# Kernel optimization log

Measured on AMD Instinct MI355X. Metric: run time of the kernel, lower is better.

Reference implementation:

```python
import jax, jax.numpy as jnp
import numpy as np

SEQ = 4096
EMB = 1024
OUT = 1024


def setup_inputs() -> dict:
    key = jax.random.key(0)
    k_x, k_q, k_k, k_v = jax.random.split(key, 4)
    scale = 1.0 / np.sqrt(EMB)
    inputs = jax.random.normal(k_x, (SEQ, EMB), dtype=jnp.float32)
    # torch Linear weight is (out_features, in_features); y = x @ W.T
    W_Q = jax.random.normal(k_q, (OUT, EMB), dtype=jnp.float32) * scale
    W_K = jax.random.normal(k_k, (OUT, EMB), dtype=jnp.float32) * scale
    W_V = jax.random.normal(k_v, (OUT, EMB), dtype=jnp.float32) * scale
    return {"inputs": inputs, "W_Q": W_Q, "W_K": W_K, "W_V": W_V}


def reference(inputs, W_Q, W_K, W_V):
    # projections: (S, E) @ (E, D) -> (S, D)
    q = inputs @ W_Q.T
    k = inputs @ W_K.T
    v = inputs @ W_V.T
    d_k = k.shape[-1]
    scores = (q @ k.T) / jnp.sqrt(jnp.asarray(d_k, dtype=q.dtype))  # (S, S)
    weights = jax.nn.softmax(scores, axis=-1)
    return weights @ v  # (S, D)
```

## Files before the change

kernel.cpp:

```cpp
#include <hip/hip_runtime.h>

typedef __bf16 bf16;
typedef __bf16 bf16x4 __attribute__((ext_vector_type(4)));
typedef __bf16 bf16x8 __attribute__((ext_vector_type(8)));
typedef float f32x4 __attribute__((ext_vector_type(4)));

#define SEQ 4096
#define EMB 1024

__device__ __forceinline__ void async_copy16(void* lds, const void* g) {
    __builtin_amdgcn_global_load_lds(
        (const __attribute__((address_space(1))) unsigned int*)g,
        (__attribute__((address_space(3))) unsigned int*)lds,
        16, 0, 0);
}

__global__ __launch_bounds__(256) void prep_all(const float* __restrict__ x,
                                                const float* __restrict__ wq,
                                                const float* __restrict__ wk,
                                                const float* __restrict__ wv,
                                                bf16* __restrict__ xb,
                                                bf16* __restrict__ wqk,
                                                bf16* __restrict__ wvb,
                                                float* __restrict__ rowsum)
{
    const int u = blockIdx.x * 256 + threadIdx.x;
    const float* src;
    bf16* dst;
    int off;
    if (u < 1048576)      { src = x;  dst = xb;               off = u; }
    else if (u < 1310720) { src = wq; dst = wqk;              off = u - 1048576; }
    else if (u < 1572864) { src = wk; dst = wqk + EMB * EMB;  off = u - 1310720; }
    else if (u < 1835008) { src = wv; dst = wvb;              off = u - 1572864; }
    else {
        *(float4*)(rowsum + (size_t)(u - 1835008) * 4) = float4{0.f, 0.f, 0.f, 0.f};
        return;
    }
    float4 f = *(const float4*)(src + (size_t)off * 4);
    bf16x4 v = { (bf16)f.x, (bf16)f.y, (bf16)f.z, (bf16)f.w };
    *(bf16x4*)(dst + (size_t)off * 4) = v;
}

template<bool RSUM>
__device__ __forceinline__ void tile_compute(const bf16* __restrict__ As,
                                             const bf16* __restrict__ Bs,
                                             int wr, int wc, int fr, int q,
                                             f32x4 (&acc)[8][4], float (&rsum)[8],
                                             bool rs_active)
{
    const int pc0 = ((q + fr) & 7) * 8;
    const int pc1 = pc0 ^ 32;

    bf16x8 bg[4][2];
#pragma unroll
    for (int nf = 0; nf < 4; nf++) {
        const bf16* bp = Bs + (wc * 64 + nf * 16 + fr) * 64;
        bg[nf][0] = *(const bf16x8*)(bp + pc0);
        bg[nf][1] = *(const bf16x8*)(bp + pc1);
    }
#pragma unroll
    for (int mg = 0; mg < 2; mg++) {
        bf16x8 af[4][2];
#pragma unroll
        for (int mf = 0; mf < 4; mf++) {
            const bf16* ap = As + (wr * 128 + mg * 64 + mf * 16 + fr) * 64;
            af[mf][0] = *(const bf16x8*)(ap + pc0);
            af[mf][1] = *(const bf16x8*)(ap + pc1);
        }
        if (RSUM && rs_active) {
#pragma unroll
            for (int mf = 0; mf < 4; mf++)
#pragma unroll
                for (int kh = 0; kh < 2; kh++)
#pragma unroll
                    for (int e = 0; e < 8; e++)
                        rsum[mg * 4 + mf] += (float)af[mf][kh][e];
        }
        __builtin_amdgcn_s_setprio(1);
#pragma unroll
        for (int nf = 0; nf < 4; nf++)
#pragma unroll
            for (int mf = 0; mf < 4; mf++) {
                f32x4 c = acc[mg * 4 + mf][nf];
                c = __builtin_amdgcn_mfma_f32_16x16x32_bf16(af[mf][0], bg[nf][0], c, 0, 0, 0);
                c = __builtin_amdgcn_mfma_f32_16x16x32_bf16(af[mf][1], bg[nf][1], c, 0, 0, 0);
                acc[mg * 4 + mf][nf] = c;
            }
        __builtin_amdgcn_s_setprio(0);
    }
}

template<bool RSUM>
__device__ __forceinline__ void gemm_core256(const bf16* __restrict__ A,
                                             const bf16* __restrict__ B,
                                             int lda, int ldb, long koff,
                                             int m0, int n0,
                                             bf16* __restrict__ As,
                                             bf16* __restrict__ Bs,
                                             f32x4 (&acc)[8][4], float (&rsum)[8],
                                             bool rs_active)
{
    const int tid  = threadIdx.x;
    const int lane = tid & 63;
    const int wave = tid >> 6;
    const int wr = wave >> 2;
    const int wc = wave & 3;
    const int srow = tid >> 3;
    const int spc  = tid & 7;
    const int sl   = (spc - (srow & 7)) & 7;
    const int fr = lane & 15;
    const int q  = lane >> 4;

#pragma unroll
    for (int i = 0; i < 8; i++)
#pragma unroll
        for (int j = 0; j < 4; j++) acc[i][j] = {0.f, 0.f, 0.f, 0.f};
    if (RSUM)
#pragma unroll
        for (int i = 0; i < 8; i++) rsum[i] = 0.f;

    const bf16* Ab = A + (size_t)(m0 + srow) * lda + koff + sl * 8;
    const bf16* Bb = B + (size_t)(n0 + srow) * ldb + koff + sl * 8;
    bf16* AsD = As + srow * 64 + spc * 8;
    bf16* BsD = Bs + srow * 64 + spc * 8;

#pragma unroll
    for (int u = 0; u < 4; u++) {
        async_copy16(AsD + u * 4096, Ab + (size_t)(64 * u) * lda);
        async_copy16(BsD + u * 4096, Bb + (size_t)(64 * u) * ldb);
    }

    for (int t = 0; t < 15; t++) {
        const int p = t & 1;
        const long kk = (long)(t + 1) * 64;
#pragma unroll
        for (int u = 0; u < 4; u++) {
            async_copy16(AsD + (1 - p) * 16384 + u * 4096, Ab + kk + (size_t)(64 * u) * lda);
            async_copy16(BsD + (1 - p) * 16384 + u * 4096, Bb + kk + (size_t)(64 * u) * ldb);
        }
        asm volatile("s_waitcnt vmcnt(8)" ::: "memory");
        __builtin_amdgcn_s_barrier();
        tile_compute<RSUM>(As + p * 16384, Bs + p * 16384, wr, wc, fr, q, acc, rsum, rs_active);
        asm volatile("" ::: "memory");
        __builtin_amdgcn_s_barrier();
    }
    asm volatile("s_waitcnt vmcnt(0)" ::: "memory");
    __builtin_amdgcn_s_barrier();
    tile_compute<RSUM>(As + 16384, Bs + 16384, wr, wc, fr, q, acc, rsum, rs_active);
}

__global__ __launch_bounds__(512, 2) void gemm_proj(const bf16* __restrict__ xb,
                                                    const bf16* __restrict__ wqk,
                                                    const bf16* __restrict__ wvb,
                                                    bf16* __restrict__ QK,
                                                    bf16* __restrict__ VT)
{
    __shared__ __align__(16) bf16 As[2][16384];
    __shared__ __align__(16) bf16 Bs[2][16384];

    const bf16 *A, *B;
    bf16* C;
    int ldc, m0, n0;
    if (blockIdx.y < 8) {
        A = xb; B = wqk; C = QK; ldc = 2048;
        m0 = blockIdx.x * 256; n0 = blockIdx.y * 256;
    } else {
        const int id = blockIdx.x + (blockIdx.y - 8) * 16;
        A = wvb; B = xb; C = VT; ldc = 4096;
        m0 = (id & 3) * 256; n0 = (id >> 2) * 256;
    }

    f32x4 acc[8][4];
    float rs[8];
    gemm_core256<false>(A, B, 1024, 1024, 0, m0, n0, &As[0][0], &Bs[0][0], acc, rs, false);

    const int lane = threadIdx.x & 63;
    const int wave = threadIdx.x >> 6;
    const int cm = m0 + (wave >> 2) * 128 + ((lane >> 4) << 2);
    const int cn = n0 + (wave & 3) * 64 + (lane & 15);
#pragma unroll
    for (int i = 0; i < 8; i++)
#pragma unroll
        for (int j = 0; j < 4; j++)
#pragma unroll
            for (int r = 0; r < 4; r++)
                C[(size_t)(cm + i * 16 + r) * ldc + (cn + j * 16)] = (bf16)acc[i][j][r];
}

__global__ __launch_bounds__(512, 2) void gemm_exp(const bf16* __restrict__ QK,
                                                   bf16* __restrict__ E)
{
    __shared__ __align__(16) bf16 As[2][16384];
    __shared__ __align__(16) bf16 Bs[2][16384];

    const int m0 = blockIdx.x * 256;
    const int n0 = blockIdx.y * 256;
    f32x4 acc[8][4];
    float rs[8];
    gemm_core256<false>(QK, QK + 1024, 2048, 2048, 0, m0, n0, &As[0][0], &Bs[0][0], acc, rs, false);

    const int lane = threadIdx.x & 63;
    const int wave = threadIdx.x >> 6;
    const int cm = m0 + (wave >> 2) * 128 + ((lane >> 4) << 2);
    const int cn = n0 + (wave & 3) * 64 + (lane & 15);
#pragma unroll
    for (int i = 0; i < 8; i++)
#pragma unroll
        for (int j = 0; j < 4; j++)
#pragma unroll
            for (int r = 0; r < 4; r++)
                E[(size_t)(cm + i * 16 + r) * 4096 + (cn + j * 16)] =
                    (bf16)__expf(acc[i][j][r] * 0.03125f);
}

__global__ __launch_bounds__(512, 2) void gemm_pv(const bf16* __restrict__ E,
                                                  const bf16* __restrict__ VT,
                                                  float* __restrict__ out,
                                                  float* __restrict__ p1,
                                                  float* __restrict__ rowsum)
{
    __shared__ __align__(16) bf16 As[2][16384];
    __shared__ __align__(16) bf16 Bs[2][16384];

    const int m0 = blockIdx.x * 256;
    const int n0 = blockIdx.y * 256;
    const long koff = (long)blockIdx.z * 1024;
    const bool rs_active = (blockIdx.y == 0) && (((threadIdx.x >> 6) & 3) == 0);

    f32x4 acc[8][4];
    float rs[8];
    gemm_core256<true>(E, VT, 4096, 4096, koff, m0, n0, &As[0][0], &Bs[0][0], acc, rs, rs_active);

    const int lane = threadIdx.x & 63;
    const int wave = threadIdx.x >> 6;
    if (rs_active) {
#pragma unroll
        for (int i = 0; i < 8; i++) {
            rs[i] += __shfl_xor(rs[i], 16);
            rs[i] += __shfl_xor(rs[i], 32);
        }
        if (lane < 16) {
            const int rbase = m0 + (wave >> 2) * 128;
#pragma unroll
            for (int i = 0; i < 8; i++)
                unsafeAtomicAdd(&rowsum[rbase + i * 16 + lane], rs[i]);
        }
    }

    float* C = (blockIdx.z == 0) ? out : p1 + (size_t)(blockIdx.z - 1) * SEQ * 1024;
    const int cm = m0 + (wave >> 2) * 128 + ((lane >> 4) << 2);
    const int cn = n0 + (wave & 3) * 64 + (lane & 15);
#pragma unroll
    for (int i = 0; i < 8; i++)
#pragma unroll
        for (int j = 0; j < 4; j++)
#pragma unroll
            for (int r = 0; r < 4; r++)
                C[(size_t)(cm + i * 16 + r) * 1024 + (cn + j * 16)] = acc[i][j][r];
}

__global__ __launch_bounds__(256) void reduce_norm(float* __restrict__ out,
                                                   const float* __restrict__ p1,
                                                   const float* __restrict__ p2,
                                                   const float* __restrict__ p3,
                                                   const float* __restrict__ rowsum)
{
    const int m = blockIdx.x;
    const float inv = 1.f / rowsum[m];
    const size_t off = (size_t)m * 1024 + threadIdx.x * 4;
    float4 a = *(const float4*)(out + off);
    float4 b = *(const float4*)(p1 + off);
    float4 c = *(const float4*)(p2 + off);
    float4 d = *(const float4*)(p3 + off);
    float4 o;
    o.x = (a.x + b.x + c.x + d.x) * inv;
    o.y = (a.y + b.y + c.y + d.y) * inv;
    o.z = (a.z + b.z + c.z + d.z) * inv;
    o.w = (a.w + b.w + c.w + d.w) * inv;
    *(float4*)(out + off) = o;
}

extern "C" void kernel_launch(void* const* d_in, const int* in_sizes, int n_in,
                              void* d_out, int out_size, void* d_ws, size_t ws_size,
                              hipStream_t stream)
{
    const float* x  = (const float*)d_in[0];
    const float* wq = (const float*)d_in[1];
    const float* wk = (const float*)d_in[2];
    const float* wv = (const float*)d_in[3];
    float* out = (float*)d_out;

    char* ws = (char*)d_ws;
    const size_t MB = 1024 * 1024;
    bf16*  E   = (bf16*)(ws);
    float* p1  = (float*)(ws + 32 * MB);
    float* p2  = (float*)(ws + 48 * MB);
    float* p3  = (float*)(ws + 64 * MB);
    bf16*  xb  = (bf16*)(ws + 32 * MB);
    bf16*  wqk = (bf16*)(ws + 40 * MB);
    bf16*  wvb = (bf16*)(ws + 44 * MB);
    bf16*  QK  = (bf16*)(ws + 64 * MB);
    bf16*  VT  = (bf16*)(ws + 80 * MB);
    float* rsm = (float*)(ws + 88 * MB);

    prep_all<<<dim3(7172), dim3(256), 0, stream>>>(x, wq, wk, wv, xb, wqk, wvb, rsm);
    gemm_proj<<<dim3(16, 12), dim3(512), 0, stream>>>(xb, wqk, wvb, QK, VT);
    gemm_exp<<<dim3(16, 16), dim3(512), 0, stream>>>(QK, E);
    gemm_pv<<<dim3(16, 4, 4), dim3(512), 0, stream>>>(E, VT, out, p1, rsm);
    reduce_norm<<<dim3(4096), dim3(256), 0, stream>>>(out, p1, p2, p3, rsm);
}
```

Measured before the change: 211.4 us.

## Split tile compute into barrier-synchronized quadrant phases with ping-pong scheduling

Restructures the per-k-tile compute into four phases that each load one A or B fragment group from LDS, then run MFMAs on one quadrant of the accumulator tile, with barriers and lgkmcnt waits between phases. The intent is to interleave LDS reads with MFMA work across the two wave groups and lower register pressure by holding only half the A and B fragments at a time. Launch bounds are relaxed from 2 to 1 blocks per CU, which allows more registers per thread but may reduce occupancy. The extra barriers per tile add synchronization overhead.

```diff
diff --git a/kernel.cpp b/kernel.cpp
--- a/kernel.cpp
+++ b/kernel.cpp
@@ -42,52 +42,125 @@
 }
 
 template<bool RSUM>
-__device__ __forceinline__ void tile_compute(const bf16* __restrict__ As,
-                                             const bf16* __restrict__ Bs,
-                                             int wr, int wc, int fr, int q,
-                                             f32x4 (&acc)[8][4], float (&rsum)[8],
-                                             bool rs_active)
+__device__ __forceinline__ void tile_phases(const bf16* __restrict__ Asp,
+                                            const bf16* __restrict__ Bsp,
+                                            int wr, int wc, int fr, int q,
+                                            f32x4 (&acc)[8][4], float (&rsum)[8],
+                                            bool rs_active)
 {
     const int pc0 = ((q + fr) & 7) * 8;
     const int pc1 = pc0 ^ 32;
-
-    bf16x8 bg[4][2];
-#pragma unroll
-    for (int nf = 0; nf < 4; nf++) {
-        const bf16* bp = Bs + (wc * 64 + nf * 16 + fr) * 64;
-        bg[nf][0] = *(const bf16x8*)(bp + pc0);
-        bg[nf][1] = *(const bf16x8*)(bp + pc1);
-    }
-#pragma unroll
-    for (int mg = 0; mg < 2; mg++) {
-        bf16x8 af[4][2];
+    const bf16* aBase = Asp + (wr * 128 + fr) * 64;
+    const bf16* bBase = Bsp + (wc * 64 + fr) * 64;
+
+    bf16x8 af[4][2];
+    bf16x8 bg[2][2][2];
+
+#pragma unroll
+    for (int mf = 0; mf < 4; mf++) {
+        af[mf][0] = *(const bf16x8*)(aBase + (mf * 16) * 64 + pc0);
+        af[mf][1] = *(const bf16x8*)(aBase + (mf * 16) * 64 + pc1);
+    }
+#pragma unroll
+    for (int nj = 0; nj < 2; nj++) {
+        bg[0][nj][0] = *(const bf16x8*)(bBase + (nj * 16) * 64 + pc0);
+        bg[0][nj][1] = *(const bf16x8*)(bBase + (nj * 16) * 64 + pc1);
+    }
+    asm volatile("" ::: "memory");
+    __builtin_amdgcn_s_barrier();
+    asm volatile("s_waitcnt lgkmcnt(0)" ::: "memory");
+    __builtin_amdgcn_sched_barrier(0);
+    __builtin_amdgcn_s_setprio(1);
+#pragma unroll
+    for (int nj = 0; nj < 2; nj++)
 #pragma unroll
         for (int mf = 0; mf < 4; mf++) {
-            const bf16* ap = As + (wr * 128 + mg * 64 + mf * 16 + fr) * 64;
-            af[mf][0] = *(const bf16x8*)(ap + pc0);
-            af[mf][1] = *(const bf16x8*)(ap + pc1);
-        }
-        if (RSUM && rs_active) {
-#pragma unroll
-            for (int mf = 0; mf < 4; mf++)
-#pragma unroll
-                for (int kh = 0; kh < 2; kh++)
-#pragma unroll
-                    for (int e = 0; e < 8; e++)
-                        rsum[mg * 4 + mf] += (float)af[mf][kh][e];
-        }
-        __builtin_amdgcn_s_setprio(1);
-#pragma unroll
-        for (int nf = 0; nf < 4; nf++)
-#pragma unroll
-            for (int mf = 0; mf < 4; mf++) {
-                f32x4 c = acc[mg * 4 + mf][nf];
-                c = __builtin_amdgcn_mfma_f32_16x16x32_bf16(af[mf][0], bg[nf][0], c, 0, 0, 0);
-                c = __builtin_amdgcn_mfma_f32_16x16x32_bf16(af[mf][1], bg[nf][1], c, 0, 0, 0);
-                acc[mg * 4 + mf][nf] = c;
-            }
-        __builtin_amdgcn_s_setprio(0);
-    }
+            f32x4 c = acc[mf][nj];
+            c = __builtin_amdgcn_mfma_f32_16x16x32_bf16(af[mf][0], bg[0][nj][0], c, 0, 0, 0);
+            c = __builtin_amdgcn_mfma_f32_16x16x32_bf16(af[mf][1], bg[0][nj][1], c, 0, 0, 0);
+            acc[mf][nj] = c;
+        }
+    __builtin_amdgcn_s_setprio(0);
+    if (RSUM && rs_active) {
+#pragma unroll
+        for (int mf = 0; mf < 4; mf++)
+#pragma unroll
+            for (int kh = 0; kh < 2; kh++)
+#pragma unroll
+                for (int e = 0; e < 8; e++)
+                    rsum[mf] += (float)af[mf][kh][e];
+    }
+    asm volatile("" ::: "memory");
+    __builtin_amdgcn_s_barrier();
+
+#pragma unroll
+    for (int nj = 0; nj < 2; nj++) {
+        bg[1][nj][0] = *(const bf16x8*)(bBase + ((2 + nj) * 16) * 64 + pc0);
+        bg[1][nj][1] = *(const bf16x8*)(bBase + ((2 + nj) * 16) * 64 + pc1);
+    }
+    asm volatile("" ::: "memory");
+    __builtin_amdgcn_s_barrier();
+    asm volatile("s_waitcnt lgkmcnt(0)" ::: "memory");
+    __builtin_amdgcn_sched_barrier(0);
+    __builtin_amdgcn_s_setprio(1);
+#pragma unroll
+    for (int nj = 0; nj < 2; nj++)
+#pragma unroll
+        for (int mf = 0; mf < 4; mf++) {
+            f32x4 c = acc[mf][2 + nj];
+            c = __builtin_amdgcn_mfma_f32_16x16x32_bf16(af[mf][0], bg[1][nj][0], c, 0, 0, 0);
+            c = __builtin_amdgcn_mfma_f32_16x16x32_bf16(af[mf][1], bg[1][nj][1], c, 0, 0, 0);
+            acc[mf][2 + nj] = c;
+        }
+    __builtin_amdgcn_s_setprio(0);
+    asm volatile("" ::: "memory");
+    __builtin_amdgcn_s_barrier();
+
+#pragma unroll
+    for (int mf = 0; mf < 4; mf++) {
+        af[mf][0] = *(const bf16x8*)(aBase + (64 + mf * 16) * 64 + pc0);
+        af[mf][1] = *(const bf16x8*)(aBase + (64 + mf * 16) * 64 + pc1);
+    }
+    asm volatile("" ::: "memory");
+    __builtin_amdgcn_s_barrier();
+    asm volatile("s_waitcnt lgkmcnt(0)" ::: "memory");
+    __builtin_amdgcn_sched_barrier(0);
+    __builtin_amdgcn_s_setprio(1);
+#pragma unroll
+    for (int nj = 0; nj < 2; nj++)
+#pragma unroll
+        for (int mf = 0; mf < 4; mf++) {
+            f32x4 c = acc[4 + mf][2 + nj];
+            c = __builtin_amdgcn_mfma_f32_16x16x32_bf16(af[mf][0], bg[1][nj][0], c, 0, 0, 0);
+            c = __builtin_amdgcn_mfma_f32_16x16x32_bf16(af[mf][1], bg[1][nj][1], c, 0, 0, 0);
+            acc[4 + mf][2 + nj] = c;
+        }
+    __builtin_amdgcn_s_setprio(0);
+    if (RSUM && rs_active) {
+#pragma unroll
+        for (int mf = 0; mf < 4; mf++)
+#pragma unroll
+            for (int kh = 0; kh < 2; kh++)
+#pragma unroll
+                for (int e = 0; e < 8; e++)
+                    rsum[4 + mf] += (float)af[mf][kh][e];
+    }
+    asm volatile("" ::: "memory");
+    __builtin_amdgcn_s_barrier();
+
+    __builtin_amdgcn_s_setprio(1);
+#pragma unroll
+    for (int nj = 0; nj < 2; nj++)
+#pragma unroll
+        for (int mf = 0; mf < 4; mf++) {
+            f32x4 c = acc[4 + mf][nj];
+            c = __builtin_amdgcn_mfma_f32_16x16x32_bf16(af[mf][0], bg[0][nj][0], c, 0, 0, 0);
+            c = __builtin_amdgcn_mfma_f32_16x16x32_bf16(af[mf][1], bg[0][nj][1], c, 0, 0, 0);
+            acc[4 + mf][nj] = c;
+        }
+    __builtin_amdgcn_s_setprio(0);
+    asm volatile("" ::: "memory");
+    __builtin_amdgcn_s_barrier();
 }
 
 template<bool RSUM>
@@ -140,16 +213,14 @@
         }
         asm volatile("s_waitcnt vmcnt(8)" ::: "memory");
         __builtin_amdgcn_s_barrier();
-        tile_compute<RSUM>(As + p * 16384, Bs + p * 16384, wr, wc, fr, q, acc, rsum, rs_active);
-        asm volatile("" ::: "memory");
-        __builtin_amdgcn_s_barrier();
+        tile_phases<RSUM>(As + p * 16384, Bs + p * 16384, wr, wc, fr, q, acc, rsum, rs_active);
     }
     asm volatile("s_waitcnt vmcnt(0)" ::: "memory");
     __builtin_amdgcn_s_barrier();
-    tile_compute<RSUM>(As + 16384, Bs + 16384, wr, wc, fr, q, acc, rsum, rs_active);
-}
-
-__global__ __launch_bounds__(512, 2) void gemm_proj(const bf16* __restrict__ xb,
+    tile_phases<RSUM>(As + 16384, Bs + 16384, wr, wc, fr, q, acc, rsum, rs_active);
+}
+
+__global__ __launch_bounds__(512, 1) void gemm_proj(const bf16* __restrict__ xb,
                                                     const bf16* __restrict__ wqk,
                                                     const bf16* __restrict__ wvb,
                                                     bf16* __restrict__ QK,
@@ -187,7 +258,7 @@
                 C[(size_t)(cm + i * 16 + r) * ldc + (cn + j * 16)] = (bf16)acc[i][j][r];
 }
 
-__global__ __launch_bounds__(512, 2) void gemm_exp(const bf16* __restrict__ QK,
+__global__ __launch_bounds__(512, 1) void gemm_exp(const bf16* __restrict__ QK,
                                                    bf16* __restrict__ E)
 {
     __shared__ __align__(16) bf16 As[2][16384];
@@ -213,7 +284,7 @@
                     (bf16)__expf(acc[i][j][r] * 0.03125f);
 }
 
-__global__ __launch_bounds__(512, 2) void gemm_pv(const bf16* __restrict__ E,
+__global__ __launch_bounds__(512, 1) void gemm_pv(const bf16* __restrict__ E,
                                                   const bf16* __restrict__ VT,
                                                   float* __restrict__ out,
                                                   float* __restrict__ p1,
```

New measurement: 226.9 us. 1.07x slower.

## Restructure GEMM mainloop into 4-stage K=32 pipeline with register ping-pong

Applied to the files above, without the earlier changes.

Replaces the double-buffered K=64 GEMM loop with a four-buffer K=32 pipeline. It prefetches two tiles ahead, splits the A and B async copies around the barrier, and double-buffers the B fragments in registers so LDS reads overlap the MFMA work. Launch bounds drop from 2 to 1 blocks per CU because shared memory use doubles. The aim is to hide global and LDS latency behind the matrix math, at the cost of occupancy and finer-grained waitcnt tuning that could stall if the counts are wrong.

```diff
diff --git a/kernel.cpp b/kernel.cpp
--- a/kernel.cpp
+++ b/kernel.cpp
@@ -42,51 +42,88 @@
 }
 
 template<bool RSUM>
-__device__ __forceinline__ void tile_compute(const bf16* __restrict__ As,
-                                             const bf16* __restrict__ Bs,
-                                             int wr, int wc, int fr, int q,
-                                             f32x4 (&acc)[8][4], float (&rsum)[8],
-                                             bool rs_active)
-{
-    const int pc0 = ((q + fr) & 7) * 8;
-    const int pc1 = pc0 ^ 32;
-
-    bf16x8 bg[4][2];
-#pragma unroll
-    for (int nf = 0; nf < 4; nf++) {
-        const bf16* bp = Bs + (wc * 64 + nf * 16 + fr) * 64;
-        bg[nf][0] = *(const bf16x8*)(bp + pc0);
-        bg[nf][1] = *(const bf16x8*)(bp + pc1);
-    }
-#pragma unroll
-    for (int mg = 0; mg < 2; mg++) {
-        bf16x8 af[4][2];
-#pragma unroll
-        for (int mf = 0; mf < 4; mf++) {
-            const bf16* ap = As + (wr * 128 + mg * 64 + mf * 16 + fr) * 64;
-            af[mf][0] = *(const bf16x8*)(ap + pc0);
-            af[mf][1] = *(const bf16x8*)(ap + pc1);
-        }
-        if (RSUM && rs_active) {
+__device__ __forceinline__ void tile_step(int t, int NT,
+                                          const bf16* __restrict__ Ab,
+                                          const bf16* __restrict__ Bb,
+                                          int lda, int ldb,
+                                          bf16* __restrict__ As,
+                                          bf16* __restrict__ Bs,
+                                          bf16* __restrict__ AsD,
+                                          bf16* __restrict__ BsD,
+                                          int wr, int wc, int fr, int pc,
+                                          bf16x8 (&afA)[4], bf16x8 (&afB)[4],
+                                          bf16x8 (&bgC)[4], bf16x8 (&bgN)[4],
+                                          f32x4 (&acc)[8][4], float (&rsum)[8],
+                                          bool rs_active)
+{
+    if (t + 2 < NT) {
+        const int b2 = ((t + 2) & 3) * 8192;
+        async_copy16(AsD + b2,        Ab + (t + 2) * 32);
+        async_copy16(AsD + b2 + 4096, Ab + (t + 2) * 32 + (size_t)128 * lda);
+    }
+    {
+        const bf16* At = As + (t & 3) * 8192 + (wr * 128 + 64 + fr) * 32 + pc;
+#pragma unroll
+        for (int mf = 0; mf < 4; mf++)
+            afB[mf] = *(const bf16x8*)(At + (mf * 16) * 32);
+    }
+    asm volatile("s_waitcnt lgkmcnt(4)" ::: "memory");
+    __builtin_amdgcn_sched_barrier(0);
+    __builtin_amdgcn_s_setprio(1);
+#pragma unroll
+    for (int nj = 0; nj < 4; nj++)
+#pragma unroll
+        for (int mf = 0; mf < 4; mf++)
+            acc[mf][nj] = __builtin_amdgcn_mfma_f32_16x16x32_bf16(afA[mf], bgC[nj], acc[mf][nj], 0, 0, 0);
+    __builtin_amdgcn_s_setprio(0);
+    if (RSUM && rs_active) {
+#pragma unroll
+        for (int mf = 0; mf < 4; mf++)
+#pragma unroll
+            for (int e = 0; e < 8; e++) rsum[mf] += (float)afA[mf][e];
+    }
+
+    if (t < NT - 1) {
+        if (t + 2 < NT) {
+            asm volatile("s_waitcnt vmcnt(2)" ::: "memory");
+        } else {
+            asm volatile("s_waitcnt vmcnt(0)" ::: "memory");
+        }
+        __builtin_amdgcn_s_barrier();
+        if (t + 2 < NT) {
+            const int b2 = ((t + 2) & 3) * 8192;
+            async_copy16(BsD + b2,        Bb + (t + 2) * 32);
+            async_copy16(BsD + b2 + 4096, Bb + (t + 2) * 32 + (size_t)128 * ldb);
+        }
+        {
+            const int b1 = ((t + 1) & 3) * 8192;
+            const bf16* At = As + b1 + (wr * 128 + fr) * 32 + pc;
+            const bf16* Bt = Bs + b1 + (wc * 64 + fr) * 32 + pc;
 #pragma unroll
             for (int mf = 0; mf < 4; mf++)
-#pragma unroll
-                for (int kh = 0; kh < 2; kh++)
-#pragma unroll
-                    for (int e = 0; e < 8; e++)
-                        rsum[mg * 4 + mf] += (float)af[mf][kh][e];
-        }
-        __builtin_amdgcn_s_setprio(1);
-#pragma unroll
-        for (int nf = 0; nf < 4; nf++)
-#pragma unroll
-            for (int mf = 0; mf < 4; mf++) {
-                f32x4 c = acc[mg * 4 + mf][nf];
-                c = __builtin_amdgcn_mfma_f32_16x16x32_bf16(af[mf][0], bg[nf][0], c, 0, 0, 0);
-                c = __builtin_amdgcn_mfma_f32_16x16x32_bf16(af[mf][1], bg[nf][1], c, 0, 0, 0);
-                acc[mg * 4 + mf][nf] = c;
-            }
-        __builtin_amdgcn_s_setprio(0);
+                afA[mf] = *(const bf16x8*)(At + (mf * 16) * 32);
+#pragma unroll
+            for (int nj = 0; nj < 4; nj++)
+                bgN[nj] = *(const bf16x8*)(Bt + (nj * 16) * 32);
+        }
+        asm volatile("s_waitcnt lgkmcnt(8)" ::: "memory");
+        __builtin_amdgcn_sched_barrier(0);
+    } else {
+        asm volatile("s_waitcnt lgkmcnt(0)" ::: "memory");
+        __builtin_amdgcn_sched_barrier(0);
+    }
+    __builtin_amdgcn_s_setprio(1);
+#pragma unroll
+    for (int nj = 0; nj < 4; nj++)
+#pragma unroll
+        for (int mf = 0; mf < 4; mf++)
+            acc[4 + mf][nj] = __builtin_amdgcn_mfma_f32_16x16x32_bf16(afB[mf], bgC[nj], acc[4 + mf][nj], 0, 0, 0);
+    __builtin_amdgcn_s_setprio(0);
+    if (RSUM && rs_active) {
+#pragma unroll
+        for (int mf = 0; mf < 4; mf++)
+#pragma unroll
+            for (int e = 0; e < 8; e++) rsum[4 + mf] += (float)afB[mf][e];
     }
 }
 
@@ -105,11 +142,13 @@
     const int wave = tid >> 6;
     const int wr = wave >> 2;
     const int wc = wave & 3;
-    const int srow = tid >> 3;
-    const int spc  = tid & 7;
-    const int sl   = (spc - (srow & 7)) & 7;
+    const int srow = tid >> 2;
+    const int spc  = tid & 3;
+    const int sl   = (spc - (srow & 3)) & 3;
     const int fr = lane & 15;
     const int q  = lane >> 4;
+    const int pc = ((q + fr) & 3) * 8;
+    const int NT = 32;
 
 #pragma unroll
     for (int i = 0; i < 8; i++)
@@ -121,42 +160,47 @@
 
     const bf16* Ab = A + (size_t)(m0 + srow) * lda + koff + sl * 8;
     const bf16* Bb = B + (size_t)(n0 + srow) * ldb + koff + sl * 8;
-    bf16* AsD = As + srow * 64 + spc * 8;
-    bf16* BsD = Bs + srow * 64 + spc * 8;
-
-#pragma unroll
-    for (int u = 0; u < 4; u++) {
-        async_copy16(AsD + u * 4096, Ab + (size_t)(64 * u) * lda);
-        async_copy16(BsD + u * 4096, Bb + (size_t)(64 * u) * ldb);
-    }
-
-    for (int t = 0; t < 15; t++) {
-        const int p = t & 1;
-        const long kk = (long)(t + 1) * 64;
-#pragma unroll
-        for (int u = 0; u < 4; u++) {
-            async_copy16(AsD + (1 - p) * 16384 + u * 4096, Ab + kk + (size_t)(64 * u) * lda);
-            async_copy16(BsD + (1 - p) * 16384 + u * 4096, Bb + kk + (size_t)(64 * u) * ldb);
-        }
-        asm volatile("s_waitcnt vmcnt(8)" ::: "memory");
-        __builtin_amdgcn_s_barrier();
-        tile_compute<RSUM>(As + p * 16384, Bs + p * 16384, wr, wc, fr, q, acc, rsum, rs_active);
-        asm volatile("" ::: "memory");
-        __builtin_amdgcn_s_barrier();
-    }
-    asm volatile("s_waitcnt vmcnt(0)" ::: "memory");
+    bf16* AsD = As + srow * 32 + spc * 8;
+    bf16* BsD = Bs + srow * 32 + spc * 8;
+
+#pragma unroll
+    for (int tt = 0; tt < 2; tt++) {
+        async_copy16(AsD + tt * 8192,        Ab + tt * 32);
+        async_copy16(AsD + tt * 8192 + 4096, Ab + tt * 32 + (size_t)128 * lda);
+        async_copy16(BsD + tt * 8192,        Bb + tt * 32);
+        async_copy16(BsD + tt * 8192 + 4096, Bb + tt * 32 + (size_t)128 * ldb);
+    }
+    asm volatile("s_waitcnt vmcnt(4)" ::: "memory");
     __builtin_amdgcn_s_barrier();
-    tile_compute<RSUM>(As + 16384, Bs + 16384, wr, wc, fr, q, acc, rsum, rs_active);
-}
-
-__global__ __launch_bounds__(512, 2) void gemm_proj(const bf16* __restrict__ xb,
+
+    bf16x8 afA[4], afB[4], bg0[4], bg1[4];
+    {
+        const bf16* At = As + (wr * 128 + fr) * 32 + pc;
+        const bf16* Bt = Bs + (wc * 64 + fr) * 32 + pc;
+#pragma unroll
+        for (int mf = 0; mf < 4; mf++)
+            afA[mf] = *(const bf16x8*)(At + (mf * 16) * 32);
+#pragma unroll
+        for (int nj = 0; nj < 4; nj++)
+            bg0[nj] = *(const bf16x8*)(Bt + (nj * 16) * 32);
+    }
+
+    for (int t = 0; t < NT; t += 2) {
+        tile_step<RSUM>(t,     NT, Ab, Bb, lda, ldb, As, Bs, AsD, BsD,
+                        wr, wc, fr, pc, afA, afB, bg0, bg1, acc, rsum, rs_active);
+        tile_step<RSUM>(t + 1, NT, Ab, Bb, lda, ldb, As, Bs, AsD, BsD,
+                        wr, wc, fr, pc, afA, afB, bg1, bg0, acc, rsum, rs_active);
+    }
+}
+
+__global__ __launch_bounds__(512, 1) void gemm_proj(const bf16* __restrict__ xb,
                                                     const bf16* __restrict__ wqk,
                                                     const bf16* __restrict__ wvb,
                                                     bf16* __restrict__ QK,
                                                     bf16* __restrict__ VT)
 {
-    __shared__ __align__(16) bf16 As[2][16384];
-    __shared__ __align__(16) bf16 Bs[2][16384];
+    __shared__ __align__(16) bf16 As[4][8192];
+    __shared__ __align__(16) bf16 Bs[4][8192];
 
     const bf16 *A, *B;
     bf16* C;
@@ -187,11 +231,11 @@
                 C[(size_t)(cm + i * 16 + r) * ldc + (cn + j * 16)] = (bf16)acc[i][j][r];
 }
 
-__global__ __launch_bounds__(512, 2) void gemm_exp(const bf16* __restrict__ QK,
+__global__ __launch_bounds__(512, 1) void gemm_exp(const bf16* __restrict__ QK,
                                                    bf16* __restrict__ E)
 {
-    __shared__ __align__(16) bf16 As[2][16384];
-    __shared__ __align__(16) bf16 Bs[2][16384];
+    __shared__ __align__(16) bf16 As[4][8192];
+    __shared__ __align__(16) bf16 Bs[4][8192];
 
     const int m0 = blockIdx.x * 256;
     const int n0 = blockIdx.y * 256;
@@ -213,14 +257,14 @@
                     (bf16)__expf(acc[i][j][r] * 0.03125f);
 }
 
-__global__ __launch_bounds__(512, 2) void gemm_pv(const bf16* __restrict__ E,
+__global__ __launch_bounds__(512, 1) void gemm_pv(const bf16* __restrict__ E,
                                                   const bf16* __restrict__ VT,
                                                   float* __restrict__ out,
                                                   float* __restrict__ p1,
                                                   float* __restrict__ rowsum)
 {
-    __shared__ __align__(16) bf16 As[2][16384];
-    __shared__ __align__(16) bf16 Bs[2][16384];
+    __shared__ __align__(16) bf16 As[4][8192];
+    __shared__ __align__(16) bf16 Bs[4][8192];
 
     const int m0 = blockIdx.x * 256;
     const int n0 = blockIdx.y * 256;
```

After: 207.9 us. Within noise of the previous version (-1.7%).

## Interleave half-tile async staging with MFMA quadrants and remap blocks per XCD

Applied to the files above, without the earlier changes.

Restructures the GEMM main loop into four MFMA quadrants per k-tile, each preceded by staging half of the next A or B tile through async LDS loads, with finer barriers and explicit waitcnt control. The goal is to overlap global-to-LDS traffic with matrix math at the granularity of a quarter tile. It also remaps block indices so that neighbouring tiles land on the same XCD for L2 reuse, and drops launch bounds occupancy from 2 to 1 block per CU. It adds more barriers per tile and lowers occupancy, trading latency hiding via extra waves for an explicit software schedule.

```diff
diff --git a/kernel.cpp b/kernel.cpp
--- a/kernel.cpp
+++ b/kernel.cpp
@@ -41,53 +41,117 @@
     *(bf16x4*)(dst + (size_t)off * 4) = v;
 }
 
-template<bool RSUM>
-__device__ __forceinline__ void tile_compute(const bf16* __restrict__ As,
-                                             const bf16* __restrict__ Bs,
-                                             int wr, int wc, int fr, int q,
-                                             f32x4 (&acc)[8][4], float (&rsum)[8],
-                                             bool rs_active)
-{
-    const int pc0 = ((q + fr) & 7) * 8;
-    const int pc1 = pc0 ^ 32;
-
-    bf16x8 bg[4][2];
-#pragma unroll
-    for (int nf = 0; nf < 4; nf++) {
-        const bf16* bp = Bs + (wc * 64 + nf * 16 + fr) * 64;
-        bg[nf][0] = *(const bf16x8*)(bp + pc0);
-        bg[nf][1] = *(const bf16x8*)(bp + pc1);
-    }
-#pragma unroll
-    for (int mg = 0; mg < 2; mg++) {
-        bf16x8 af[4][2];
+__device__ __forceinline__ void stage_half(bf16* lbase, const bf16* gbase,
+                                           int ldx, int t, int h) {
+    const bf16* g = gbase + t * 64 + (size_t)(h * 128) * ldx;
+    bf16* l = lbase + h * 8192;
+    async_copy16(l,        g);
+    async_copy16(l + 4096, g + (size_t)64 * ldx);
+}
+
+__device__ __forceinline__ void quad_mfma(bf16x8 (&af)[4][2], bf16x8 (&bg)[2][2],
+                                          f32x4 (&acc)[8][4], int mg, int ngh)
+{
+#pragma unroll
+    for (int nj = 0; nj < 2; nj++)
 #pragma unroll
         for (int mf = 0; mf < 4; mf++) {
-            const bf16* ap = As + (wr * 128 + mg * 64 + mf * 16 + fr) * 64;
-            af[mf][0] = *(const bf16x8*)(ap + pc0);
-            af[mf][1] = *(const bf16x8*)(ap + pc1);
+            f32x4 c = acc[mg * 4 + mf][ngh * 2 + nj];
+            c = __builtin_amdgcn_mfma_f32_16x16x32_bf16(af[mf][0], bg[nj][0], c, 0, 0, 0);
+            c = __builtin_amdgcn_mfma_f32_16x16x32_bf16(af[mf][1], bg[nj][1], c, 0, 0, 0);
+            acc[mg * 4 + mf][ngh * 2 + nj] = c;
         }
-        if (RSUM && rs_active) {
-#pragma unroll
-            for (int mf = 0; mf < 4; mf++)
-#pragma unroll
-                for (int kh = 0; kh < 2; kh++)
-#pragma unroll
-                    for (int e = 0; e < 8; e++)
-                        rsum[mg * 4 + mf] += (float)af[mf][kh][e];
-        }
-        __builtin_amdgcn_s_setprio(1);
-#pragma unroll
-        for (int nf = 0; nf < 4; nf++)
-#pragma unroll
-            for (int mf = 0; mf < 4; mf++) {
-                f32x4 c = acc[mg * 4 + mf][nf];
-                c = __builtin_amdgcn_mfma_f32_16x16x32_bf16(af[mf][0], bg[nf][0], c, 0, 0, 0);
-                c = __builtin_amdgcn_mfma_f32_16x16x32_bf16(af[mf][1], bg[nf][1], c, 0, 0, 0);
-                acc[mg * 4 + mf][nf] = c;
-            }
-        __builtin_amdgcn_s_setprio(0);
-    }
+}
+
+__device__ __forceinline__ void rsum_add(bf16x8 (&af)[4][2], float (&rsum)[8], int mg)
+{
+#pragma unroll
+    for (int mf = 0; mf < 4; mf++)
+#pragma unroll
+        for (int kh = 0; kh < 2; kh++)
+#pragma unroll
+            for (int e = 0; e < 8; e++)
+                rsum[mg * 4 + mf] += (float)af[mf][kh][e];
+}
+
+template<bool RSUM, bool STGA, bool STGB, int VMN>
+__device__ __forceinline__ void group4(int g,
+    const bf16* Ard, const bf16* Brd,
+    bf16* AwH, bf16* BwH,
+    const bf16* Ab, const bf16* Bb, int lda, int ldb,
+    int wr, int wc, int fr, int pc0, int pc1,
+    f32x4 (&acc)[8][4], float (&rsum)[8], bool rs_active)
+{
+    bf16x8 af[4][2], bg0[2][2], bg1[2][2];
+    const bf16* Arow = Ard + (wr * 128 + fr) * 64;
+    const bf16* Brow = Brd + (wc * 64 + fr) * 64;
+
+    if (STGA) stage_half(AwH, Ab, lda, g + 1, 0);
+#pragma unroll
+    for (int mf = 0; mf < 4; mf++) {
+        af[mf][0] = *(const bf16x8*)(Arow + mf * 1024 + pc0);
+        af[mf][1] = *(const bf16x8*)(Arow + mf * 1024 + pc1);
+    }
+#pragma unroll
+    for (int nj = 0; nj < 2; nj++) {
+        bg0[nj][0] = *(const bf16x8*)(Brow + nj * 1024 + pc0);
+        bg0[nj][1] = *(const bf16x8*)(Brow + nj * 1024 + pc1);
+    }
+    asm volatile("" ::: "memory");
+    __builtin_amdgcn_s_barrier();
+    asm volatile("s_waitcnt lgkmcnt(0)" ::: "memory");
+    __builtin_amdgcn_sched_barrier(0);
+    __builtin_amdgcn_s_setprio(1);
+    quad_mfma(af, bg0, acc, 0, 0);
+    __builtin_amdgcn_s_setprio(0);
+    if (RSUM && rs_active) rsum_add(af, rsum, 0);
+    asm volatile("" ::: "memory");
+    __builtin_amdgcn_s_barrier();
+
+    if (STGA) stage_half(AwH, Ab, lda, g + 1, 1);
+#pragma unroll
+    for (int nj = 0; nj < 2; nj++) {
+        bg1[nj][0] = *(const bf16x8*)(Brow + (2 + nj) * 1024 + pc0);
+        bg1[nj][1] = *(const bf16x8*)(Brow + (2 + nj) * 1024 + pc1);
+    }
+    asm volatile("" ::: "memory");
+    __builtin_amdgcn_s_barrier();
+    asm volatile("s_waitcnt lgkmcnt(0)" ::: "memory");
+    __builtin_amdgcn_sched_barrier(0);
+    __builtin_amdgcn_s_setprio(1);
+    quad_mfma(af, bg1, acc, 0, 1);
+    __builtin_amdgcn_s_setprio(0);
+    asm volatile("" ::: "memory");
+    __builtin_amdgcn_s_barrier();
+
+    if (STGB) stage_half(BwH, Bb, ldb, g + 2, 0);
+#pragma unroll
+    for (int mf = 0; mf < 4; mf++) {
+        af[mf][0] = *(const bf16x8*)(Arow + 4096 + mf * 1024 + pc0);
+        af[mf][1] = *(const bf16x8*)(Arow + 4096 + mf * 1024 + pc1);
+    }
+    asm volatile("" ::: "memory");
+    __builtin_amdgcn_s_barrier();
+    asm volatile("s_waitcnt lgkmcnt(0)" ::: "memory");
+    __builtin_amdgcn_sched_barrier(0);
+    __builtin_amdgcn_s_setprio(1);
+    quad_mfma(af, bg1, acc, 1, 1);
+    __builtin_amdgcn_s_setprio(0);
+    if (RSUM && rs_active) rsum_add(af, rsum, 1);
+    asm volatile("" ::: "memory");
+    __builtin_amdgcn_s_barrier();
+
+    if (STGB) stage_half(BwH, Bb, ldb, g + 2, 1);
+    if constexpr (VMN == 4) { asm volatile("s_waitcnt vmcnt(4)" ::: "memory"); }
+    else if constexpr (VMN == 0) { asm volatile("s_waitcnt vmcnt(0)" ::: "memory"); }
+    asm volatile("" ::: "memory");
+    __builtin_amdgcn_s_barrier();
+    __builtin_amdgcn_sched_barrier(0);
+    __builtin_amdgcn_s_setprio(1);
+    quad_mfma(af, bg0, acc, 1, 0);
+    __builtin_amdgcn_s_setprio(0);
+    asm volatile("" ::: "memory");
+    __builtin_amdgcn_s_barrier();
 }
 
 template<bool RSUM>
@@ -110,6 +174,8 @@
     const int sl   = (spc - (srow & 7)) & 7;
     const int fr = lane & 15;
     const int q  = lane >> 4;
+    const int pc0 = ((q + fr) & 7) * 8;
+    const int pc1 = pc0 ^ 32;
 
 #pragma unroll
     for (int i = 0; i < 8; i++)
@@ -121,35 +187,37 @@
 
     const bf16* Ab = A + (size_t)(m0 + srow) * lda + koff + sl * 8;
     const bf16* Bb = B + (size_t)(n0 + srow) * ldb + koff + sl * 8;
-    bf16* AsD = As + srow * 64 + spc * 8;
-    bf16* BsD = Bs + srow * 64 + spc * 8;
-
-#pragma unroll
-    for (int u = 0; u < 4; u++) {
-        async_copy16(AsD + u * 4096, Ab + (size_t)(64 * u) * lda);
-        async_copy16(BsD + u * 4096, Bb + (size_t)(64 * u) * ldb);
-    }
-
-    for (int t = 0; t < 15; t++) {
-        const int p = t & 1;
-        const long kk = (long)(t + 1) * 64;
-#pragma unroll
-        for (int u = 0; u < 4; u++) {
-            async_copy16(AsD + (1 - p) * 16384 + u * 4096, Ab + kk + (size_t)(64 * u) * lda);
-            async_copy16(BsD + (1 - p) * 16384 + u * 4096, Bb + kk + (size_t)(64 * u) * ldb);
-        }
-        asm volatile("s_waitcnt vmcnt(8)" ::: "memory");
-        __builtin_amdgcn_s_barrier();
-        tile_compute<RSUM>(As + p * 16384, Bs + p * 16384, wr, wc, fr, q, acc, rsum, rs_active);
-        asm volatile("" ::: "memory");
-        __builtin_amdgcn_s_barrier();
-    }
-    asm volatile("s_waitcnt vmcnt(0)" ::: "memory");
-    __builtin_amdgcn_s_barrier();
-    tile_compute<RSUM>(As + 16384, Bs + 16384, wr, wc, fr, q, acc, rsum, rs_active);
-}
-
-__global__ __launch_bounds__(512, 2) void gemm_proj(const bf16* __restrict__ xb,
+    const int soff = srow * 64 + spc * 8;
+
+    stage_half(As + soff,         Ab, lda, 0, 0);
+    stage_half(As + soff,         Ab, lda, 0, 1);
+    stage_half(Bs + soff,         Bb, ldb, 0, 0);
+    stage_half(Bs + soff,         Bb, ldb, 0, 1);
+    stage_half(Bs + 16384 + soff, Bb, ldb, 1, 0);
+    stage_half(Bs + 16384 + soff, Bb, ldb, 1, 1);
+    asm volatile("s_waitcnt vmcnt(4)" ::: "memory");
+    __builtin_amdgcn_s_barrier();
+
+    for (int gg = 0; gg < 7; gg++) {
+        const int g0 = 2 * gg;
+        group4<RSUM, true, true, 4>(g0, As, Bs, As + 16384 + soff, Bs + soff,
+                                    Ab, Bb, lda, ldb, wr, wc, fr, pc0, pc1,
+                                    acc, rsum, rs_active);
+        group4<RSUM, true, true, 4>(g0 + 1, As + 16384, Bs + 16384,
+                                    As + soff, Bs + 16384 + soff,
+                                    Ab, Bb, lda, ldb, wr, wc, fr, pc0, pc1,
+                                    acc, rsum, rs_active);
+    }
+    group4<RSUM, true, false, 0>(14, As, Bs, As + 16384 + soff, Bs + soff,
+                                 Ab, Bb, lda, ldb, wr, wc, fr, pc0, pc1,
+                                 acc, rsum, rs_active);
+    group4<RSUM, false, false, -1>(15, As + 16384, Bs + 16384,
+                                   As + soff, Bs + 16384 + soff,
+                                   Ab, Bb, lda, ldb, wr, wc, fr, pc0, pc1,
+                                   acc, rsum, rs_active);
+}
+
+__global__ __launch_bounds__(512, 1) void gemm_proj(const bf16* __restrict__ xb,
                                                     const bf16* __restrict__ wqk,
                                                     const bf16* __restrict__ wvb,
                                                     bf16* __restrict__ QK,
@@ -158,14 +226,20 @@
     __shared__ __align__(16) bf16 As[2][16384];
     __shared__ __align__(16) bf16 Bs[2][16384];
 
+    const int hw  = blockIdx.x + 16 * blockIdx.y;
+    const int xcd = hw & 7;
+    const int s   = hw >> 3;
+    const int bx  = ((xcd & 1) << 3) | (s & 7);
+    const int byy = (xcd >> 1) * 3 + (s >> 3);
+
     const bf16 *A, *B;
     bf16* C;
     int ldc, m0, n0;
-    if (blockIdx.y < 8) {
+    if (byy < 8) {
         A = xb; B = wqk; C = QK; ldc = 2048;
-        m0 = blockIdx.x * 256; n0 = blockIdx.y * 256;
+        m0 = bx * 256; n0 = byy * 256;
     } else {
-        const int id = blockIdx.x + (blockIdx.y - 8) * 16;
+        const int id = bx + (byy - 8) * 16;
         A = wvb; B = xb; C = VT; ldc = 4096;
         m0 = (id & 3) * 256; n0 = (id >> 2) * 256;
     }
@@ -187,14 +261,20 @@
                 C[(size_t)(cm + i * 16 + r) * ldc + (cn + j * 16)] = (bf16)acc[i][j][r];
 }
 
-__global__ __launch_bounds__(512, 2) void gemm_exp(const bf16* __restrict__ QK,
+__global__ __launch_bounds__(512, 1) void gemm_exp(const bf16* __restrict__ QK,
                                                    bf16* __restrict__ E)
 {
     __shared__ __align__(16) bf16 As[2][16384];
     __shared__ __align__(16) bf16 Bs[2][16384];
 
-    const int m0 = blockIdx.x * 256;
-    const int n0 = blockIdx.y * 256;
+    const int hw  = blockIdx.x + 16 * blockIdx.y;
+    const int xcd = hw & 7;
+    const int s   = hw >> 3;
+    const int bx  = ((xcd & 1) << 3) | (s & 7);
+    const int by  = ((xcd >> 1) << 2) | (s >> 3);
+
+    const int m0 = bx * 256;
+    const int n0 = by * 256;
     f32x4 acc[8][4];
     float rs[8];
     gemm_core256<false>(QK, QK + 1024, 2048, 2048, 0, m0, n0, &As[0][0], &Bs[0][0], acc, rs, false);
@@ -213,7 +293,7 @@
                     (bf16)__expf(acc[i][j][r] * 0.03125f);
 }
 
-__global__ __launch_bounds__(512, 2) void gemm_pv(const bf16* __restrict__ E,
+__global__ __launch_bounds__(512, 1) void gemm_pv(const bf16* __restrict__ E,
                                                   const bf16* __restrict__ VT,
                                                   float* __restrict__ out,
                                                   float* __restrict__ p1,
@@ -222,10 +302,17 @@
     __shared__ __align__(16) bf16 As[2][16384];
     __shared__ __align__(16) bf16 Bs[2][16384];
 
-    const int m0 = blockIdx.x * 256;
-    const int n0 = blockIdx.y * 256;
-    const long koff = (long)blockIdx.z * 1024;
-    const bool rs_active = (blockIdx.y == 0) && (((threadIdx.x >> 6) & 3) == 0);
+    const int hw  = blockIdx.x + 16 * blockIdx.y + 64 * blockIdx.z;
+    const int xcd = hw & 7;
+    const int s   = hw >> 3;
+    const int bx  = ((xcd & 1) << 3) | (s & 7);
+    const int by  = s >> 3;
+    const int bz  = xcd >> 1;
+
+    const int m0 = bx * 256;
+    const int n0 = by * 256;
+    const long koff = (long)bz * 1024;
+    const bool rs_active = (by == 0) && (((threadIdx.x >> 6) & 3) == 0);
 
     f32x4 acc[8][4];
     float rs[8];
@@ -247,7 +334,7 @@
         }
     }
 
-    float* C = (blockIdx.z == 0) ? out : p1 + (size_t)(blockIdx.z - 1) * SEQ * 1024;
+    float* C = (bz == 0) ? out : p1 + (size_t)(bz - 1) * SEQ * 1024;
     const int cm = m0 + (wave >> 2) * 128 + ((lane >> 4) << 2);
     const int cn = n0 + (wave & 3) * 64 + (lane & 15);
 #pragma unroll
```

New measurement: 209.7 us. About the same (-0.8%).
